# Kernel optimization log

Measured on AMD Instinct MI355X. Metric: run time of the kernel, lower is better.

Reference implementation:

```python
import jax, jax.numpy as jnp
import numpy as np

N, E = 50000, 1600000
D_IN, D_OUT = 256, 64
ALPHA = 0.2        # LeakyReLU slope used on attention logits (self.leakyrelu)
BT_SLOPE = 0.01    # F.leaky_relu default slope inside relu_bt


def _xavier_normal(key, shape, gain):
    fan_in, fan_out = shape[0], shape[1]
    std = gain * np.sqrt(2.0 / (fan_in + fan_out))
    return jax.random.normal(key, shape, dtype=jnp.float32) * std


def relu_bt(x):
    # -threshold(-leaky_relu(x), -t, -t) == min(leaky_relu(x), t), t = ||x||_inf (detached)
    t = jax.lax.stop_gradient(jnp.max(jnp.abs(x)))
    y = jnp.where(x >= 0, x, BT_SLOPE * x)
    return jnp.minimum(y, t)


def setup_inputs() -> dict:
    key = jax.random.key(0)
    k0, k1, k2, k3, k4, k5 = jax.random.split(key, 6)
    inp = jax.random.normal(k0, (N, D_IN), dtype=jnp.float32)
    edge = jax.random.randint(k1, (2, E), 0, N, dtype=jnp.int64)
    W_high = _xavier_normal(k2, (D_IN, D_OUT), 1.414)
    W_low = _xavier_normal(k3, (D_IN, D_OUT), 1.414)
    a_high = _xavier_normal(k4, (1, D_OUT), 1.414)
    a_low = _xavier_normal(k5, (1, D_OUT), 1.414)
    return {"input": inp, "edge": edge, "W_high": W_high, "W_low": W_low,
            "a_high": a_high, "a_low": a_low}


def reference(input, edge, W_high, W_low, a_high, a_low):
    n = input.shape[0]
    src, dst = edge[0], edge[1]

    h_high = relu_bt(input @ W_high)  # [N, D_OUT]
    h_low = relu_bt(input @ W_low)    # [N, D_OUT]

    # a @ (h[src] -/+ h[dst])^T == (a.h)[src] -/+ (a.h)[dst]: compute per-node scalar
    # projections first, then gather scalars per edge (avoids [E, D_OUT] edge features).
    s_high = h_high @ a_high[0]       # [N]
    s_low = h_low @ a_low[0]          # [N]

    def lrelu(x):
        return jnp.where(x >= 0, x, ALPHA * x)

    edge_e_high = jnp.exp(-lrelu(s_high[src] - s_high[dst]))  # [E]
    edge_e_low = jnp.exp(-lrelu(s_low[src] + s_low[dst]))     # [E]
    # dropout p=0.0 -> identity

    # sparse A @ ones -> per-row sum of attention weights
    rowsum_high = jax.ops.segment_sum(edge_e_high, src, num_segments=n)[:, None]
    rowsum_low = jax.ops.segment_sum(edge_e_low, src, num_segments=n)[:, None]

    # sparse A @ h -> weighted aggregation of neighbor features
    hp_high = jax.ops.segment_sum(edge_e_high[:, None] * h_high[dst], src, num_segments=n)
    hp_low = jax.ops.segment_sum(edge_e_low[:, None] * h_low[dst], src, num_segments=n)

    hp_high = hp_high / (rowsum_high + 1e-16)
    hp_low = hp_low / (rowsum_low + 1e-16)

    # concat=True branch
    return relu_bt(jnp.concatenate([hp_high, hp_low], axis=1))  # [N, 2*D_OUT]
```

## Files before the change

### kernel.cpp

```cpp
#include <hip/hip_runtime.h>
#include <hip/hip_bf16.h>
#include <cstdint>

#define NN    50000
#define NE    1600000
#define DIN   256
#define DOUT  64
#define CAPS  96
#define CAPD  95

#define BKT   196
#define BCAP  10240
#define EPB   4096
#define EPT   16
#define NBIN  391
#define MTB   64
#define NGEMM 782

typedef __attribute__((ext_vector_type(8))) short frag8;
typedef __attribute__((ext_vector_type(4))) float fragc;

union PK { __hip_bfloat162 b2; uint32_t u; };
union CH { frag8 v; uint32_t u[4]; };

__device__ __forceinline__ float leaky01(float x) { return x >= 0.f ? x : 0.01f * x; }

__device__ __forceinline__ uint32_t pk2(float lo, float hi) {
  PK p; p.b2 = __float22bfloat162_rn(make_float2(lo, hi)); return p.u;
}

__device__ __forceinline__ int   bcast_i(int v, int lane) {
  return __builtin_amdgcn_readlane(v, lane);
}

__device__ __forceinline__ float bfH(uint32_t u) { return __uint_as_float(u << 16); }
__device__ __forceinline__ float bfL(uint32_t u) { return __uint_as_float(u & 0xffff0000u); }

__global__ __launch_bounds__(256) void prep_kernel(
    const float* __restrict__ Wh, const float* __restrict__ Wl,
    __hip_bfloat16* __restrict__ Wt, int* __restrict__ cursor)
{
  if (blockIdx.x == 0 && threadIdx.x < BKT) cursor[threadIdx.x] = 0;
  int g = blockIdx.x * 256 + threadIdx.x;
  if (g < 2 * DOUT * DIN) {
    int m = g >> 14, rem = g & 16383;
    int n = rem >> 8, k = rem & 255;
    float v = (m ? Wl : Wh)[k * DOUT + n];
    Wt[g] = __float2bfloat16(v);
  }
}

__global__ __launch_bounds__(256) void fused_kernel(
    const float* __restrict__ inp, const __hip_bfloat16* __restrict__ Wt,
    const float* __restrict__ ah, const float* __restrict__ al,
    const int* __restrict__ edge, int* __restrict__ cursor,
    uint32_t* __restrict__ binned, uint32_t* __restrict__ HL,
    float2* __restrict__ ss)
{
  __shared__ __align__(16) char smem[32768];

  const int idx = blockIdx.x;
  const int t = threadIdx.x;

  if (idx < NBIN) {
    uint32_t* stage  = (uint32_t*)smem;
    int*      hist   = (int*)(smem + 16384);
    int*      cur    = (int*)(smem + 17408);
    int*      base_g = (int*)(smem + 18192);
    int*      scan_s = (int*)(smem + 18976);

    const int e0 = idx * EPB;
    uint32_t v[EPT];
#pragma unroll
    for (int i = 0; i < EPT; i++) {
      int e = e0 + i * 256 + t;
      if (e < NE) {
        uint32_t s = (uint32_t)edge[e];
        uint32_t d = (uint32_t)edge[NE + e];
        v[i] = (s << 16) | d;
      } else {
        v[i] = 0xFFFFFFFFu;
      }
    }
    if (t < 256) hist[t] = 0;
    for (int b = t; b < BKT; b += 256) cur[b] = 0;
    __syncthreads();
#pragma unroll
    for (int i = 0; i < EPT; i++) {
      int b = v[i] >> 24;
      if (b < BKT) atomicAdd(&hist[b], 1);
    }
    __syncthreads();
    if (t < 64) {
      int carry = 0;
#pragma unroll
      for (int seg = 0; seg < 4; seg++) {
        int i = seg * 64 + t;
        int h = hist[i];
        int s = h;
#pragma unroll
        for (int off = 1; off < 64; off <<= 1) {
          int o = __shfl_up(s, off);
          if (t >= off) s += o;
        }
        int excl = carry + s - h;
        if (i <= BKT) scan_s[i] = excl;
        carry += bcast_i(s, 63);
      }
    }
    __syncthreads();
    for (int b = t; b < BKT; b += 256) {
      int h = hist[b];
      base_g[b] = h ? atomicAdd(&cursor[b], h) : 0;
    }
    __syncthreads();
#pragma unroll
    for (int i = 0; i < EPT; i++) {
      int b = v[i] >> 24;
      if (b < BKT) {
        int pos = atomicAdd(&cur[b], 1);
        stage[scan_s[b] + pos] = v[i];
      }
    }
    __syncthreads();
    const int total = scan_s[BKT];
    for (int i = t; i < total; i += 256) {
      uint32_t sv = stage[i];
      int bb = sv >> 24;
      int ofs = base_g[bb] + (i - scan_s[bb]);
      if (ofs < BCAP) binned[(size_t)bb * BCAP + ofs] = sv;
    }
    return;
  }

  const int gid = idx - NBIN;
  const int n0 = gid * MTB;
  const int lane = t & 63;
  const int w = t >> 6;
  const int quad = lane >> 4, nn = lane & 15;

  const frag8* Wt8 = (const frag8*)Wt;
  const int bbase = ((w * 16 + nn) << 5) + quad;
  frag8 bH[8], bL[8];
#pragma unroll
  for (int q = 0; q < 8; q++) {
    bH[q] = Wt8[bbase + (q << 2)];
    bL[q] = Wt8[2048 + bbase + (q << 2)];
  }

  const float4* inp4 = (const float4*)inp;
  const int l5 = t & 31;
  const int rw = t >> 5;
  {
    const int q8 = l5 >> 2, qd = l5 & 3;
#pragma unroll
    for (int i = 0; i < 8; i++) {
      int row = i * 8 + rw;
      int node = n0 + row;
      float4 a0 = make_float4(0.f, 0.f, 0.f, 0.f), a1 = a0;
      if (node < NN) {
        a0 = inp4[(size_t)node * 64 + l5 * 2];
        a1 = inp4[(size_t)node * 64 + l5 * 2 + 1];
      }
      int c = ((row >> 4) << 9) | (q8 << 6) | (qd << 4) | (row & 15);
      int B = c << 4;
      B ^= ((B >> 8) & 7) << 4;
      CH ch;
      ch.u[0] = pk2(a0.x, a0.y);
      ch.u[1] = pk2(a0.z, a0.w);
      ch.u[2] = pk2(a1.x, a1.y);
      ch.u[3] = pk2(a1.z, a1.w);
      *(frag8*)(smem + B) = ch.v;
    }
  }
  __syncthreads();

  fragc accH[4], accL[4];
#pragma unroll
  for (int m = 0; m < 4; m++) {
    accH[m] = (fragc){0.f, 0.f, 0.f, 0.f};
    accL[m] = (fragc){0.f, 0.f, 0.f, 0.f};
  }

#pragma unroll
  for (int q = 0; q < 8; q++) {
#pragma unroll
    for (int mt = 0; mt < 4; mt++) {
      int R = (mt << 13) + (q << 10) + (lane << 4);
      R ^= ((R >> 8) & 7) << 4;
      frag8 af = *(const frag8*)(smem + R);
      accH[mt] = __builtin_amdgcn_mfma_f32_16x16x32_bf16(af, bH[q], accH[mt], 0, 0, 0);
      accL[mt] = __builtin_amdgcn_mfma_f32_16x16x32_bf16(af, bL[q], accL[mt], 0, 0, 0);
    }
  }
  __syncthreads();

  float* sred = (float*)smem;
  const float ahv = ah[w * 16 + nn];
  const float alv = al[w * 16 + nn];
#pragma unroll
  for (int mt = 0; mt < 4; mt++) {
#pragma unroll
    for (int r = 0; r < 4; r++) {
      int rowb = (mt << 4) + (quad << 2) + r;
      int node = n0 + rowb;
      float hH = leaky01(accH[mt][r]);
      float hL = leaky01(accL[mt][r]);
      if (node < NN) HL[(size_t)node * DOUT + w * 16 + nn] = pk2(hH, hL);
      float pH = hH * ahv, pL = hL * alv;
#pragma unroll
      for (int off = 1; off < 16; off <<= 1) {
        pH += __shfl_xor(pH, off);
        pL += __shfl_xor(pL, off);
      }
      if (nn == 0) {
        sred[rowb * 8 + w]     = pH;
        sred[rowb * 8 + 4 + w] = pL;
      }
    }
  }
  __syncthreads();
  if (t < 64) {
    int node = n0 + t;
    if (node < NN) {
      float sH = sred[t * 8 + 0] + sred[t * 8 + 1] + sred[t * 8 + 2] + sred[t * 8 + 3];
      float sL = sred[t * 8 + 4] + sred[t * 8 + 5] + sred[t * 8 + 6] + sred[t * 8 + 7];
      ss[node] = make_float2(sH, sL);
    }
  }
}

__global__ __launch_bounds__(256) void csr_kernel(
    const uint32_t* __restrict__ binned, const int* __restrict__ cursor,
    int* __restrict__ col)
{
  __shared__ int lst[64][CAPS];
  __shared__ int cnt[64];
  const int blk = blockIdx.x;
  const int b    = ((blk >> 5) << 3) + (blk & 7);
  const int part = (blk >> 3) & 3;
  if (b >= BKT) return;
  const int t = threadIdx.x;
  if (t < 64) cnt[t] = 0;
  __syncthreads();
  int n = cursor[b]; if (n > BCAP) n = BCAP;
  const uint32_t* eb = binned + (size_t)b * BCAP;
  for (int i = t; i < n; i += 256) {
    uint32_t v = eb[i];
    int src = v >> 16, dst = v & 0xffff;
    int loc = src & 255;
    if ((loc >> 6) == part) {
      int pos = atomicAdd(&cnt[loc & 63], 1);
      if (pos < CAPD) lst[loc & 63][1 + pos] = dst;
    }
  }
  __syncthreads();
  if (t < 64) {
    int c = cnt[t]; if (c > CAPD) c = CAPD;
    lst[t][0] = c;
  }
  __syncthreads();
  const int base_node = (b << 8) + (part << 6);
  int4* dst4 = (int4*)(col + (size_t)base_node * CAPS);
  const int4* src4 = (const int4*)&lst[0][0];
  for (int i = t; i < 64 * CAPS / 4; i += 256) {
    int node = base_node + i / (CAPS / 4);
    if (node < NN) dst4[i] = src4[i];
  }
}

__global__ __launch_bounds__(256) void agg_kernel(
    const uint32_t* __restrict__ HL, const float2* __restrict__ ss,
    const int* __restrict__ col, float* __restrict__ out)
{
  int wave = (blockIdx.x * blockDim.x + threadIdx.x) >> 6;
  int lane = threadIdx.x & 63;
  if (wave >= NN) return;
  const int n = wave;
  const int* cl = col + (size_t)n * CAPS;
  int d = cl[0]; if (d > CAPD) d = CAPD;

  const float2 sn = ss[n];
  const uint2* HL2 = (const uint2*)HL;

  const int vodd4 = (lane & 32) >> 3;
  const int lo31  = lane & 31;

  float accH0 = 0.f, accH1 = 0.f, accL0 = 0.f, accL1 = 0.f;
  float rsH = 0.f, rsL = 0.f;

  for (int base = 0; base < d; base += 64) {
    int m = d - base; if (m > 64) m = 64;
    int   dst_l = 0;
    float eh_l = 0.f, el_l = 0.f;
    if (lane < m) {
      dst_l = cl[1 + base + lane];
      float2 sd = ss[dst_l];
      float xh = sn.x - sd.x;
      xh = (xh >= 0.f) ? xh : 0.2f * xh;
      eh_l = __expf(-xh);
      float xl = sn.y + sd.y;
      xl = (xl >= 0.f) ? xl : 0.2f * xl;
      el_l = __expf(-xl);
    }
    const int ehb = __float_as_int(eh_l);
    const int elb = __float_as_int(el_l);
    const int pj = (m + 1) >> 1;
    for (int jj = 0; jj < pj; jj += 4) {
      int vdd[4]; float veh[4], vel[4]; uint2 u[4];
#pragma unroll
      for (int x = 0; x < 4; x++) {
        int ib = vodd4 + ((jj + x) << 3);
        vdd[x] = __builtin_amdgcn_ds_bpermute(ib, dst_l);
        veh[x] = __int_as_float(__builtin_amdgcn_ds_bpermute(ib, ehb));
        vel[x] = __int_as_float(__builtin_amdgcn_ds_bpermute(ib, elb));
      }
#pragma unroll
      for (int x = 0; x < 4; x++)
        u[x] = HL2[(((uint32_t)vdd[x]) << 5) + lo31];
#pragma unroll
      for (int x = 0; x < 4; x++) {
        accH0 += veh[x] * bfH(u[x].x);
        accL0 += vel[x] * bfL(u[x].x);
        accH1 += veh[x] * bfH(u[x].y);
        accL1 += vel[x] * bfL(u[x].y);
      }
    }
    float rh = eh_l, rl = el_l;
#pragma unroll
    for (int off = 1; off < 64; off <<= 1) {
      rh += __shfl_xor(rh, off);
      rl += __shfl_xor(rl, off);
    }
    rsH += rh; rsL += rl;
  }

  accH0 += __shfl_xor(accH0, 32);
  accH1 += __shfl_xor(accH1, 32);
  accL0 += __shfl_xor(accL0, 32);
  accL1 += __shfl_xor(accL1, 32);

  float r  = (lane < 32) ? rsH : rsL;
  float a0 = (lane < 32) ? accH0 : accL0;
  float a1 = (lane < 32) ? accH1 : accL1;
  float inv = 1.f / (r + 1e-16f);
  float o0 = leaky01(a0 * inv);
  float o1 = leaky01(a1 * inv);
  float2* op = (float2*)(out + (size_t)n * 128 + ((lane & 32) << 1) + (lo31 << 1));
  *op = make_float2(o0, o1);
}

extern "C" void kernel_launch(void* const* d_in, const int* in_sizes, int n_in,
                              void* d_out, int out_size, void* d_ws, size_t ws_size,
                              hipStream_t stream) {
  const float* inp  = (const float*)d_in[0];
  const int*   edge = (const int*)d_in[1];
  const float* Wh   = (const float*)d_in[2];
  const float* Wl   = (const float*)d_in[3];
  const float* ah   = (const float*)d_in[4];
  const float* al   = (const float*)d_in[5];
  float* out = (float*)d_out;

  char* ws = (char*)d_ws;
  uint32_t* HL     = (uint32_t*)(ws + 0);
  float2*   ss     = (float2*)  (ws + 12800000);
  int*      col    = (int*)     (ws + 13200000);
  uint32_t* binned = (uint32_t*)(ws + 32400000);
  int*      cursor = (int*)     (ws + 40428160);
  __hip_bfloat16* Wt = (__hip_bfloat16*)(ws + 13200000);

  prep_kernel<<<128, 256, 0, stream>>>(Wh, Wl, Wt, cursor);
  fused_kernel<<<NBIN + NGEMM, 256, 0, stream>>>(inp, Wt, ah, al, edge,
                                                 cursor, binned, HL, ss);
  csr_kernel<<<800, 256, 0, stream>>>(binned, cursor, col);
  agg_kernel<<<NN / 4, 256, 0, stream>>>(HL, ss, col, out);
}
```

Measured before the change: 196.3 us.

## Partition neighbor lists by destination range and aggregate in global passes

The CSR build now splits each node's neighbor list into four segments by destination-ID range, with the per-segment counts packed into the header word. The aggregation kernel gives each wave 13 nodes and runs four passes, one per destination range, so that at any moment all waves gather from the same slice of the feature table, which is meant to improve L2/MALL locality. The cost is 13×6 accumulator arrays per lane, extra header decoding, a second pass over the binned edges in the CSR kernel, and possible load imbalance from the fixed grid of 1024 blocks. Waves are not synchronized with each other, so the passes may drift apart and lose the intended locality.

```diff
diff --git a/kernel.cpp b/kernel.cpp
--- a/kernel.cpp
+++ b/kernel.cpp
@@ -16,6 +16,11 @@
 #define NBIN  391
 #define MTB   64
 #define NGEMM 782
+
+#define PASSN 4
+#define PDIV  12500
+#define ABLK  1024
+#define NPN   13
 
 typedef __attribute__((ext_vector_type(8))) short frag8;
 typedef __attribute__((ext_vector_type(4))) float fragc;
@@ -235,13 +240,14 @@
     int* __restrict__ col)
 {
   __shared__ int lst[64][CAPS];
-  __shared__ int cnt[64];
+  __shared__ int cnt4[64][4];
+  __shared__ int cur4[64][4];
   const int blk = blockIdx.x;
   const int b    = ((blk >> 5) << 3) + (blk & 7);
   const int part = (blk >> 3) & 3;
   if (b >= BKT) return;
   const int t = threadIdx.x;
-  if (t < 64) cnt[t] = 0;
+  if (t < 256) { ((int*)cnt4)[t] = 0; ((int*)cur4)[t] = 0; }
   __syncthreads();
   int n = cursor[b]; if (n > BCAP) n = BCAP;
   const uint32_t* eb = binned + (size_t)b * BCAP;
@@ -249,15 +255,31 @@
     uint32_t v = eb[i];
     int src = v >> 16, dst = v & 0xffff;
     int loc = src & 255;
+    if ((loc >> 6) == part) atomicAdd(&cnt4[loc & 63][dst / PDIV], 1);
+  }
+  __syncthreads();
+  if (t < 64) {
+    int c0 = cnt4[t][0], c1 = cnt4[t][1], c2 = cnt4[t][2], c3 = cnt4[t][3];
+    int C0 = min(c0, CAPD);
+    int C1 = min(c0 + c1, CAPD) - C0;
+    int C2 = min(c0 + c1 + c2, CAPD) - C0 - C1;
+    int C3 = min(c0 + c1 + c2 + c3, CAPD) - C0 - C1 - C2;
+    lst[t][0] = C0 | (C1 << 8) | (C2 << 16) | (C3 << 24);
+    cur4[t][0] = 0;            cnt4[t][0] = C0;
+    cur4[t][1] = C0;           cnt4[t][1] = C0 + C1;
+    cur4[t][2] = C0 + C1;      cnt4[t][2] = C0 + C1 + C2;
+    cur4[t][3] = C0 + C1 + C2; cnt4[t][3] = C0 + C1 + C2 + C3;
+  }
+  __syncthreads();
+  for (int i = t; i < n; i += 256) {
+    uint32_t v = eb[i];
+    int src = v >> 16, dst = v & 0xffff;
+    int loc = src & 255;
     if ((loc >> 6) == part) {
-      int pos = atomicAdd(&cnt[loc & 63], 1);
-      if (pos < CAPD) lst[loc & 63][1 + pos] = dst;
-    }
-  }
-  __syncthreads();
-  if (t < 64) {
-    int c = cnt[t]; if (c > CAPD) c = CAPD;
-    lst[t][0] = c;
+      int nd = loc & 63, seg = dst / PDIV;
+      int pos = atomicAdd(&cur4[nd][seg], 1);
+      if (pos < cnt4[nd][seg]) lst[nd][1 + pos] = dst;
+    }
   }
   __syncthreads();
   const int base_node = (b << 8) + (part << 6);
@@ -269,85 +291,104 @@
   }
 }
 
-__global__ __launch_bounds__(256) void agg_kernel(
+__global__ __launch_bounds__(256, 4) void agg_kernel(
     const uint32_t* __restrict__ HL, const float2* __restrict__ ss,
     const int* __restrict__ col, float* __restrict__ out)
 {
-  int wave = (blockIdx.x * blockDim.x + threadIdx.x) >> 6;
-  int lane = threadIdx.x & 63;
-  if (wave >= NN) return;
-  const int n = wave;
-  const int* cl = col + (size_t)n * CAPS;
-  int d = cl[0]; if (d > CAPD) d = CAPD;
-
-  const float2 sn = ss[n];
+  const int W = blockIdx.x * 4 + (threadIdx.x >> 6);
+  const int lane = threadIdx.x & 63;
   const uint2* HL2 = (const uint2*)HL;
-
   const int vodd4 = (lane & 32) >> 3;
   const int lo31  = lane & 31;
-
-  float accH0 = 0.f, accH1 = 0.f, accL0 = 0.f, accL1 = 0.f;
-  float rsH = 0.f, rsL = 0.f;
-
-  for (int base = 0; base < d; base += 64) {
-    int m = d - base; if (m > 64) m = 64;
-    int   dst_l = 0;
-    float eh_l = 0.f, el_l = 0.f;
-    if (lane < m) {
-      dst_l = cl[1 + base + lane];
-      float2 sd = ss[dst_l];
-      float xh = sn.x - sd.x;
-      xh = (xh >= 0.f) ? xh : 0.2f * xh;
-      eh_l = __expf(-xh);
-      float xl = sn.y + sd.y;
-      xl = (xl >= 0.f) ? xl : 0.2f * xl;
-      el_l = __expf(-xl);
-    }
-    const int ehb = __float_as_int(eh_l);
-    const int elb = __float_as_int(el_l);
-    const int pj = (m + 1) >> 1;
-    for (int jj = 0; jj < pj; jj += 4) {
-      int vdd[4]; float veh[4], vel[4]; uint2 u[4];
-#pragma unroll
-      for (int x = 0; x < 4; x++) {
-        int ib = vodd4 + ((jj + x) << 3);
-        vdd[x] = __builtin_amdgcn_ds_bpermute(ib, dst_l);
-        veh[x] = __int_as_float(__builtin_amdgcn_ds_bpermute(ib, ehb));
-        vel[x] = __int_as_float(__builtin_amdgcn_ds_bpermute(ib, elb));
-      }
-#pragma unroll
-      for (int x = 0; x < 4; x++)
-        u[x] = HL2[(((uint32_t)vdd[x]) << 5) + lo31];
-#pragma unroll
-      for (int x = 0; x < 4; x++) {
-        accH0 += veh[x] * bfH(u[x].x);
-        accL0 += vel[x] * bfL(u[x].x);
-        accH1 += veh[x] * bfH(u[x].y);
-        accL1 += vel[x] * bfL(u[x].y);
-      }
-    }
-    float rh = eh_l, rl = el_l;
-#pragma unroll
-    for (int off = 1; off < 64; off <<= 1) {
-      rh += __shfl_xor(rh, off);
-      rl += __shfl_xor(rl, off);
-    }
-    rsH += rh; rsL += rl;
-  }
-
-  accH0 += __shfl_xor(accH0, 32);
-  accH1 += __shfl_xor(accH1, 32);
-  accL0 += __shfl_xor(accL0, 32);
-  accL1 += __shfl_xor(accL1, 32);
-
-  float r  = (lane < 32) ? rsH : rsL;
-  float a0 = (lane < 32) ? accH0 : accL0;
-  float a1 = (lane < 32) ? accH1 : accL1;
-  float inv = 1.f / (r + 1e-16f);
-  float o0 = leaky01(a0 * inv);
-  float o1 = leaky01(a1 * inv);
-  float2* op = (float2*)(out + (size_t)n * 128 + ((lane & 32) << 1) + (lo31 << 1));
-  *op = make_float2(o0, o1);
+  const int nbase = W * NPN;
+
+  float aH0[NPN], aH1[NPN], aL0[NPN], aL1[NPN], rH[NPN], rL[NPN];
+#pragma unroll
+  for (int i = 0; i < NPN; i++) {
+    aH0[i] = 0.f; aH1[i] = 0.f; aL0[i] = 0.f; aL1[i] = 0.f;
+    rH[i] = 0.f;  rL[i] = 0.f;
+  }
+
+  for (int pass = 0; pass < PASSN; pass++) {
+#pragma unroll
+    for (int i = 0; i < NPN; i++) {
+      int n = nbase + i;
+      if (n >= NN) continue;
+      const int* cl = col + (size_t)n * CAPS;
+      int pc = cl[0];
+      int m = (pc >> (8 * pass)) & 255;
+      if (m == 0) continue;
+      int off = 1;
+      if (pass > 0) off += pc & 255;
+      if (pass > 1) off += (pc >> 8) & 255;
+      if (pass > 2) off += (pc >> 16) & 255;
+      const float2 sn = ss[n];
+
+      for (int base = 0; base < m; base += 64) {
+        int mm = m - base; if (mm > 64) mm = 64;
+        int   dst_l = 0;
+        float eh_l = 0.f, el_l = 0.f;
+        if (lane < mm) {
+          dst_l = cl[off + base + lane];
+          float2 sd = ss[dst_l];
+          float xh = sn.x - sd.x;
+          xh = (xh >= 0.f) ? xh : 0.2f * xh;
+          eh_l = __expf(-xh);
+          float xl = sn.y + sd.y;
+          xl = (xl >= 0.f) ? xl : 0.2f * xl;
+          el_l = __expf(-xl);
+        }
+        const int ehb = __float_as_int(eh_l);
+        const int elb = __float_as_int(el_l);
+        const int pj = (mm + 1) >> 1;
+        for (int jj = 0; jj < pj; jj += 4) {
+          int vdd[4]; float veh[4], vel[4]; uint2 u[4];
+#pragma unroll
+          for (int x = 0; x < 4; x++) {
+            int ib = vodd4 + ((jj + x) << 3);
+            vdd[x] = __builtin_amdgcn_ds_bpermute(ib, dst_l);
+            veh[x] = __int_as_float(__builtin_amdgcn_ds_bpermute(ib, ehb));
+            vel[x] = __int_as_float(__builtin_amdgcn_ds_bpermute(ib, elb));
+          }
+#pragma unroll
+          for (int x = 0; x < 4; x++)
+            u[x] = HL2[(((uint32_t)vdd[x]) << 5) + lo31];
+#pragma unroll
+          for (int x = 0; x < 4; x++) {
+            aH0[i] += veh[x] * bfH(u[x].x);
+            aL0[i] += vel[x] * bfL(u[x].x);
+            aH1[i] += veh[x] * bfH(u[x].y);
+            aL1[i] += vel[x] * bfL(u[x].y);
+          }
+        }
+        float rh = eh_l, rl = el_l;
+#pragma unroll
+        for (int off2 = 1; off2 < 64; off2 <<= 1) {
+          rh += __shfl_xor(rh, off2);
+          rl += __shfl_xor(rl, off2);
+        }
+        rH[i] += rh; rL[i] += rl;
+      }
+    }
+  }
+
+#pragma unroll
+  for (int i = 0; i < NPN; i++) {
+    int n = nbase + i;
+    if (n >= NN) continue;
+    float h0 = aH0[i] + __shfl_xor(aH0[i], 32);
+    float h1 = aH1[i] + __shfl_xor(aH1[i], 32);
+    float l0 = aL0[i] + __shfl_xor(aL0[i], 32);
+    float l1 = aL1[i] + __shfl_xor(aL1[i], 32);
+    float r  = (lane < 32) ? rH[i] : rL[i];
+    float a0 = (lane < 32) ? h0 : l0;
+    float a1 = (lane < 32) ? h1 : l1;
+    float inv = 1.f / (r + 1e-16f);
+    float o0 = leaky01(a0 * inv);
+    float o1 = leaky01(a1 * inv);
+    float2* op = (float2*)(out + (size_t)n * 128 + ((lane & 32) << 1) + (lo31 << 1));
+    *op = make_float2(o0, o1);
+  }
 }
 
 extern "C" void kernel_launch(void* const* d_in, const int* in_sizes, int n_in,
@@ -373,5 +414,5 @@
   fused_kernel<<<NBIN + NGEMM, 256, 0, stream>>>(inp, Wt, ah, al, edge,
                                                  cursor, binned, HL, ss);
   csr_kernel<<<800, 256, 0, stream>>>(binned, cursor, col);
-  agg_kernel<<<NN / 4, 256, 0, stream>>>(HL, ss, col, out);
-}
+  agg_kernel<<<ABLK, 256, 0, stream>>>(HL, ss, col, out);
+}
```

Result: slower. 311.7 us (+58.8%).
